# Kernel optimization log

Hardware: AMD Instinct MI355X
Metric: run time of the kernel (lower is better)

The kernel has to match this reference:

```python
import jax, jax.numpy as jnp
import numpy as np

D_TENSOR = 64  # matches init_kwargs; note: original divides scores by d_tensor (not sqrt)


def setup_inputs() -> dict:
    key = jax.random.key(0)
    kq, kk, kv = jax.random.split(key, 3)
    shape = (2, 12, 2048, 64)  # [B, H, S, D]
    return {
        "queries": jax.random.normal(kq, shape, dtype=jnp.float32),
        "keys": jax.random.normal(kk, shape, dtype=jnp.float32),
        "values": jax.random.normal(kv, shape, dtype=jnp.float32),
    }


def reference(queries, keys, values):
    # scores: [B, H, S, S]; faithful to source: divide by d_tensor (NOT sqrt)
    scores = jnp.einsum("bhqd,bhkd->bhqk", queries, keys) / D_TENSOR
    attn = jax.nn.softmax(scores, axis=-1)
    out = jnp.einsum("bhqk,bhkd->bhqd", attn, values)
    return (out, attn)
```

## Files before the change

kernel.cpp:

```cpp
#include <hip/hip_runtime.h>
#include <hip/hip_bf16.h>

namespace {

constexpr int S = 2048;
constexpr int D = 64;
constexpr int BH = 24;
constexpr int QT = 64;
constexpr int KT = 64;
constexpr int NKT = S / KT;
constexpr int PAD = 72;

typedef __attribute__((ext_vector_type(8))) __bf16 bf16x8;
typedef __attribute__((ext_vector_type(4))) __bf16 bf16x4;
typedef __attribute__((ext_vector_type(4))) float  f32x4;

__device__ inline bf16x4 cvt4(f32x4 f) {
    return __builtin_convertvector(f, bf16x4);
}

__global__ __launch_bounds__(256, 5)
void rowsum_kernel(const float* __restrict__ q,
                   const float* __restrict__ k,
                   float* __restrict__ invrs) {
    __shared__ unsigned short Ks[2][KT][PAD];
    __shared__ unsigned short QPs[QT][PAD];

    const int tid  = threadIdx.x;
    const int wid  = tid >> 6;
    const int lane = tid & 63;
    const int g    = lane >> 4;
    const int r16  = lane & 15;
    const int bh   = blockIdx.y;
    const int q0   = blockIdx.x * QT;

    const float* qg = q + ((size_t)bh * S + q0) * D;
    const float* kg = k + (size_t)bh * S * D;

    #pragma unroll
    for (int ii = 0; ii < 4; ++ii) {
        int idx = tid + ii * 256;
        int r = idx >> 4, c = (idx & 15) * 4;
        f32x4 f = *reinterpret_cast<const f32x4*>(qg + r * D + c);
        *reinterpret_cast<bf16x4*>(&QPs[r][c]) = cvt4(f);
    }
    __syncthreads();
    const bf16x8 bQ0 = *(const bf16x8*)&QPs[wid * 16 + r16][g * 8];
    const bf16x8 bQ1 = *(const bf16x8*)&QPs[wid * 16 + r16][32 + g * 8];

    float rs0 = 0.f, rs1 = 0.f;
    f32x4 pK[4];

    #pragma unroll
    for (int ii = 0; ii < 4; ++ii) {
        int idx = tid + ii * 256;
        int r = idx >> 4, c = (idx & 15) * 4;
        pK[ii] = *reinterpret_cast<const f32x4*>(kg + r * D + c);
    }
    #pragma unroll
    for (int ii = 0; ii < 4; ++ii) {
        int idx = tid + ii * 256;
        int r = idx >> 4, c = (idx & 15) * 4;
        *reinterpret_cast<bf16x4*>(&Ks[0][r][c]) = cvt4(pK[ii]);
    }
    __syncthreads();

    for (int t = 0; t < NKT; ++t) {
        const int cur = t & 1;
        if (t + 1 < NKT) {
            const float* ktg = kg + (size_t)(t + 1) * KT * D;
            #pragma unroll
            for (int ii = 0; ii < 4; ++ii) {
                int idx = tid + ii * 256;
                int r = idx >> 4, c = (idx & 15) * 4;
                pK[ii] = *reinterpret_cast<const f32x4*>(ktg + r * D + c);
            }
        }
        #pragma unroll
        for (int cf = 0; cf < 4; ++cf) {
            bf16x8 aK0 = *(const bf16x8*)&Ks[cur][cf * 16 + r16][g * 8];
            bf16x8 aK1 = *(const bf16x8*)&Ks[cur][cf * 16 + r16][32 + g * 8];
            f32x4 acc = {0.f, 0.f, 0.f, 0.f};
            acc = __builtin_amdgcn_mfma_f32_16x16x32_bf16(aK0, bQ0, acc, 0, 0, 0);
            acc = __builtin_amdgcn_mfma_f32_16x16x32_bf16(aK1, bQ1, acc, 0, 0, 0);
            rs0 += __expf(acc[0] * (1.0f / 64.0f)) + __expf(acc[2] * (1.0f / 64.0f));
            rs1 += __expf(acc[1] * (1.0f / 64.0f)) + __expf(acc[3] * (1.0f / 64.0f));
        }
        if (t + 1 < NKT) {
            const int nxt = (t + 1) & 1;
            #pragma unroll
            for (int ii = 0; ii < 4; ++ii) {
                int idx = tid + ii * 256;
                int r = idx >> 4, c = (idx & 15) * 4;
                *reinterpret_cast<bf16x4*>(&Ks[nxt][r][c]) = cvt4(pK[ii]);
            }
            __syncthreads();
        }
    }
    float rs = rs0 + rs1;
    rs += __shfl_xor(rs, 16, 64);
    rs += __shfl_xor(rs, 32, 64);
    if (lane < 16)
        invrs[(size_t)bh * S + q0 + wid * 16 + lane] = 1.0f / rs;
}

__global__ __launch_bounds__(256, 5)
void attn_pv_kernel(const float* __restrict__ q,
                    const float* __restrict__ k,
                    const float* __restrict__ v,
                    const float* __restrict__ invrs,
                    float* __restrict__ out,
                    float* __restrict__ attn) {
    __shared__ unsigned short Ks[KT][PAD];
    __shared__ unsigned short Vt[D][PAD];
    __shared__ unsigned short QPs[QT][PAD];

    const int tid  = threadIdx.x;
    const int wid  = tid >> 6;
    const int lane = tid & 63;
    const int g    = lane >> 4;
    const int r16  = lane & 15;
    const int bh   = blockIdx.y;
    const int q0   = blockIdx.x * QT;

    const float* qg = q + ((size_t)bh * S + q0) * D;
    const float* kg = k + (size_t)bh * S * D;
    const float* vg = v + (size_t)bh * S * D;
    float* attng = attn + ((size_t)bh * S + q0) * S;
    float* outg  = out  + ((size_t)bh * S + q0) * D;

    #pragma unroll
    for (int ii = 0; ii < 4; ++ii) {
        int idx = tid + ii * 256;
        int r = idx >> 4, c = (idx & 15) * 4;
        f32x4 f = *reinterpret_cast<const f32x4*>(qg + r * D + c);
        *reinterpret_cast<bf16x4*>(&QPs[r][c]) = cvt4(f);
    }
    __syncthreads();
    const bf16x8 bQ0 = *(const bf16x8*)&QPs[wid * 16 + r16][g * 8];
    const bf16x8 bQ1 = *(const bf16x8*)&QPs[wid * 16 + r16][32 + g * 8];

    const float inv = invrs[(size_t)bh * S + q0 + wid * 16 + r16];

    f32x4 oacc[4];
    #pragma unroll
    for (int n = 0; n < 4; ++n) oacc[n] = {0.f, 0.f, 0.f, 0.f};

    f32x4 pK[4], pV[4];
    const int vk0 = (tid & 15) * 4;
    const int vc  = (tid >> 4) * 4;

    #pragma unroll
    for (int ii = 0; ii < 4; ++ii) {
        int idx = tid + ii * 256;
        int r = idx >> 4, c = (idx & 15) * 4;
        pK[ii] = *reinterpret_cast<const f32x4*>(kg + r * D + c);
        pV[ii] = *reinterpret_cast<const f32x4*>(vg + (vk0 + ii) * D + vc);
    }
    #pragma unroll
    for (int ii = 0; ii < 4; ++ii) {
        int idx = tid + ii * 256;
        int r = idx >> 4, c = (idx & 15) * 4;
        *reinterpret_cast<bf16x4*>(&Ks[r][c]) = cvt4(pK[ii]);
    }
    #pragma unroll
    for (int j = 0; j < 4; ++j) {
        f32x4 col = { pV[0][j], pV[1][j], pV[2][j], pV[3][j] };
        *reinterpret_cast<bf16x4*>(&Vt[vc + j][vk0]) = cvt4(col);
    }
    __syncthreads();

    for (int t = 0; t < NKT; ++t) {
        if (t + 1 < NKT) {
            const float* ktg = kg + (size_t)(t + 1) * KT * D;
            const float* vtg = vg + (size_t)(t + 1) * KT * D;
            #pragma unroll
            for (int ii = 0; ii < 4; ++ii) {
                int idx = tid + ii * 256;
                int r = idx >> 4, c = (idx & 15) * 4;
                pK[ii] = *reinterpret_cast<const f32x4*>(ktg + r * D + c);
                pV[ii] = *reinterpret_cast<const f32x4*>(vtg + (vk0 + ii) * D + vc);
            }
        }
        #pragma unroll
        for (int cf = 0; cf < 4; ++cf) {
            bf16x8 aK0 = *(const bf16x8*)&Ks[cf * 16 + r16][g * 8];
            bf16x8 aK1 = *(const bf16x8*)&Ks[cf * 16 + r16][32 + g * 8];
            f32x4 acc = {0.f, 0.f, 0.f, 0.f};
            acc = __builtin_amdgcn_mfma_f32_16x16x32_bf16(aK0, bQ0, acc, 0, 0, 0);
            acc = __builtin_amdgcn_mfma_f32_16x16x32_bf16(aK1, bQ1, acc, 0, 0, 0);
            f32x4 pst;
            #pragma unroll
            for (int e = 0; e < 4; ++e)
                pst[e] = __expf(acc[e] * (1.0f / 64.0f)) * inv;
            __builtin_nontemporal_store(pst, reinterpret_cast<f32x4*>(
                attng + (size_t)(wid * 16 + r16) * S + t * KT + cf * 16 + g * 4));
            *reinterpret_cast<bf16x4*>(&QPs[wid * 16 + r16][cf * 16 + g * 4]) = cvt4(pst);
        }
        bf16x8 aP0 = *(const bf16x8*)&QPs[wid * 16 + r16][g * 8];
        bf16x8 aP1 = *(const bf16x8*)&QPs[wid * 16 + r16][32 + g * 8];
        #pragma unroll
        for (int n = 0; n < 4; ++n) {
            bf16x8 bv0 = *(const bf16x8*)&Vt[n * 16 + r16][g * 8];
            bf16x8 bv1 = *(const bf16x8*)&Vt[n * 16 + r16][32 + g * 8];
            oacc[n] = __builtin_amdgcn_mfma_f32_16x16x32_bf16(aP0, bv0, oacc[n], 0, 0, 0);
            oacc[n] = __builtin_amdgcn_mfma_f32_16x16x32_bf16(aP1, bv1, oacc[n], 0, 0, 0);
        }
        if (t + 1 < NKT) {
            __syncthreads();
            #pragma unroll
            for (int ii = 0; ii < 4; ++ii) {
                int idx = tid + ii * 256;
                int r = idx >> 4, c = (idx & 15) * 4;
                *reinterpret_cast<bf16x4*>(&Ks[r][c]) = cvt4(pK[ii]);
            }
            #pragma unroll
            for (int j = 0; j < 4; ++j) {
                f32x4 col = { pV[0][j], pV[1][j], pV[2][j], pV[3][j] };
                *reinterpret_cast<bf16x4*>(&Vt[vc + j][vk0]) = cvt4(col);
            }
            __syncthreads();
        }
    }

    #pragma unroll
    for (int n = 0; n < 4; ++n) {
        #pragma unroll
        for (int e = 0; e < 4; ++e) {
            __builtin_nontemporal_store(oacc[n][e],
                outg + (size_t)(wid * 16 + g * 4 + e) * D + n * 16 + r16);
        }
    }
}

__global__ __launch_bounds__(256, 3)
void sdpa_fallback(const float* __restrict__ q,
                   const float* __restrict__ k,
                   const float* __restrict__ v,
                   float* __restrict__ out,
                   float* __restrict__ attn) {
    __shared__ unsigned short Ks[2][KT][PAD];
    __shared__ unsigned short Vt[2][D][PAD];
    __shared__ unsigned short QPs[QT][PAD];

    const int tid  = threadIdx.x;
    const int wid  = tid >> 6;
    const int lane = tid & 63;
    const int g    = lane >> 4;
    const int r16  = lane & 15;
    const int bh   = blockIdx.y;
    const int q0   = blockIdx.x * QT;

    const float* qg = q + ((size_t)bh * S + q0) * D;
    const float* kg = k + (size_t)bh * S * D;
    const float* vg = v + (size_t)bh * S * D;
    float* attng = attn + ((size_t)bh * S + q0) * S;
    float* outg  = out  + ((size_t)bh * S + q0) * D;

    #pragma unroll
    for (int ii = 0; ii < 4; ++ii) {
        int idx = tid + ii * 256;
        int r = idx >> 4, c = (idx & 15) * 4;
        f32x4 f = *reinterpret_cast<const f32x4*>(qg + r * D + c);
        *reinterpret_cast<bf16x4*>(&QPs[r][c]) = cvt4(f);
    }
    __syncthreads();
    const bf16x8 bQ0 = *(const bf16x8*)&QPs[wid * 16 + r16][g * 8];
    const bf16x8 bQ1 = *(const bf16x8*)&QPs[wid * 16 + r16][32 + g * 8];

    float rs = 0.0f;
    f32x4 pK[4];

    #pragma unroll
    for (int ii = 0; ii < 4; ++ii) {
        int idx = tid + ii * 256;
        int r = idx >> 4, c = (idx & 15) * 4;
        pK[ii] = *reinterpret_cast<const f32x4*>(kg + r * D + c);
    }
    #pragma unroll
    for (int ii = 0; ii < 4; ++ii) {
        int idx = tid + ii * 256;
        int r = idx >> 4, c = (idx & 15) * 4;
        *reinterpret_cast<bf16x4*>(&Ks[0][r][c]) = cvt4(pK[ii]);
    }
    __syncthreads();

    for (int t = 0; t < NKT; ++t) {
        const int cur = t & 1;
        if (t + 1 < NKT) {
            const float* ktg = kg + (size_t)(t + 1) * KT * D;
            #pragma unroll
            for (int ii = 0; ii < 4; ++ii) {
                int idx = tid + ii * 256;
                int r = idx >> 4, c = (idx & 15) * 4;
                pK[ii] = *reinterpret_cast<const f32x4*>(ktg + r * D + c);
            }
        }
        #pragma unroll
        for (int cf = 0; cf < 4; ++cf) {
            bf16x8 aK0 = *(const bf16x8*)&Ks[cur][cf * 16 + r16][g * 8];
            bf16x8 aK1 = *(const bf16x8*)&Ks[cur][cf * 16 + r16][32 + g * 8];
            f32x4 acc = {0.f, 0.f, 0.f, 0.f};
            acc = __builtin_amdgcn_mfma_f32_16x16x32_bf16(aK0, bQ0, acc, 0, 0, 0);
            acc = __builtin_amdgcn_mfma_f32_16x16x32_bf16(aK1, bQ1, acc, 0, 0, 0);
            #pragma unroll
            for (int e = 0; e < 4; ++e)
                rs += __expf(acc[e] * (1.0f / 64.0f));
        }
        if (t + 1 < NKT) {
            const int nxt = (t + 1) & 1;
            #pragma unroll
            for (int ii = 0; ii < 4; ++ii) {
                int idx = tid + ii * 256;
                int r = idx >> 4, c = (idx & 15) * 4;
                *reinterpret_cast<bf16x4*>(&Ks[nxt][r][c]) = cvt4(pK[ii]);
            }
            __syncthreads();
        }
    }
    rs += __shfl_xor(rs, 16, 64);
    rs += __shfl_xor(rs, 32, 64);
    const float inv = 1.0f / rs;

    f32x4 oacc[4];
    #pragma unroll
    for (int n = 0; n < 4; ++n) oacc[n] = {0.f, 0.f, 0.f, 0.f};

    f32x4 pV[4];
    const int vk0 = (tid & 15) * 4;
    const int vc  = (tid >> 4) * 4;

    #pragma unroll
    for (int ii = 0; ii < 4; ++ii) {
        int idx = tid + ii * 256;
        int r = idx >> 4, c = (idx & 15) * 4;
        pK[ii] = *reinterpret_cast<const f32x4*>(kg + r * D + c);
        pV[ii] = *reinterpret_cast<const f32x4*>(vg + (vk0 + ii) * D + vc);
    }
    #pragma unroll
    for (int ii = 0; ii < 4; ++ii) {
        int idx = tid + ii * 256;
        int r = idx >> 4, c = (idx & 15) * 4;
        *reinterpret_cast<bf16x4*>(&Ks[0][r][c]) = cvt4(pK[ii]);
    }
    #pragma unroll
    for (int j = 0; j < 4; ++j) {
        f32x4 col = { pV[0][j], pV[1][j], pV[2][j], pV[3][j] };
        *reinterpret_cast<bf16x4*>(&Vt[0][vc + j][vk0]) = cvt4(col);
    }
    __syncthreads();

    for (int t = 0; t < NKT; ++t) {
        const int cur = t & 1;
        if (t + 1 < NKT) {
            const float* ktg = kg + (size_t)(t + 1) * KT * D;
            const float* vtg = vg + (size_t)(t + 1) * KT * D;
            #pragma unroll
            for (int ii = 0; ii < 4; ++ii) {
                int idx = tid + ii * 256;
                int r = idx >> 4, c = (idx & 15) * 4;
                pK[ii] = *reinterpret_cast<const f32x4*>(ktg + r * D + c);
                pV[ii] = *reinterpret_cast<const f32x4*>(vtg + (vk0 + ii) * D + vc);
            }
        }
        #pragma unroll
        for (int cf = 0; cf < 4; ++cf) {
            bf16x8 aK0 = *(const bf16x8*)&Ks[cur][cf * 16 + r16][g * 8];
            bf16x8 aK1 = *(const bf16x8*)&Ks[cur][cf * 16 + r16][32 + g * 8];
            f32x4 acc = {0.f, 0.f, 0.f, 0.f};
            acc = __builtin_amdgcn_mfma_f32_16x16x32_bf16(aK0, bQ0, acc, 0, 0, 0);
            acc = __builtin_amdgcn_mfma_f32_16x16x32_bf16(aK1, bQ1, acc, 0, 0, 0);
            f32x4 pst;
            #pragma unroll
            for (int e = 0; e < 4; ++e)
                pst[e] = __expf(acc[e] * (1.0f / 64.0f)) * inv;
            __builtin_nontemporal_store(pst, reinterpret_cast<f32x4*>(
                attng + (size_t)(wid * 16 + r16) * S + t * KT + cf * 16 + g * 4));
            *reinterpret_cast<bf16x4*>(&QPs[wid * 16 + r16][cf * 16 + g * 4]) = cvt4(pst);
        }
        bf16x8 aP0 = *(const bf16x8*)&QPs[wid * 16 + r16][g * 8];
        bf16x8 aP1 = *(const bf16x8*)&QPs[wid * 16 + r16][32 + g * 8];
        #pragma unroll
        for (int n = 0; n < 4; ++n) {
            bf16x8 bv0 = *(const bf16x8*)&Vt[cur][n * 16 + r16][g * 8];
            bf16x8 bv1 = *(const bf16x8*)&Vt[cur][n * 16 + r16][32 + g * 8];
            oacc[n] = __builtin_amdgcn_mfma_f32_16x16x32_bf16(aP0, bv0, oacc[n], 0, 0, 0);
            oacc[n] = __builtin_amdgcn_mfma_f32_16x16x32_bf16(aP1, bv1, oacc[n], 0, 0, 0);
        }
        if (t + 1 < NKT) {
            const int nxt = (t + 1) & 1;
            #pragma unroll
            for (int ii = 0; ii < 4; ++ii) {
                int idx = tid + ii * 256;
                int r = idx >> 4, c = (idx & 15) * 4;
                *reinterpret_cast<bf16x4*>(&Ks[nxt][r][c]) = cvt4(pK[ii]);
            }
            #pragma unroll
            for (int j = 0; j < 4; ++j) {
                f32x4 col = { pV[0][j], pV[1][j], pV[2][j], pV[3][j] };
                *reinterpret_cast<bf16x4*>(&Vt[nxt][vc + j][vk0]) = cvt4(col);
            }
            __syncthreads();
        }
    }

    #pragma unroll
    for (int n = 0; n < 4; ++n) {
        #pragma unroll
        for (int e = 0; e < 4; ++e) {
            __builtin_nontemporal_store(oacc[n][e],
                outg + (size_t)(wid * 16 + g * 4 + e) * D + n * 16 + r16);
        }
    }
}

}

extern "C" void kernel_launch(void* const* d_in, const int* in_sizes, int n_in,
                              void* d_out, int out_size, void* d_ws, size_t ws_size,
                              hipStream_t stream) {
    const float* q = (const float*)d_in[0];
    const float* k = (const float*)d_in[1];
    const float* v = (const float*)d_in[2];
    float* out  = (float*)d_out;
    float* attn = out + (size_t)BH * S * D;

    constexpr size_t RS_BYTES = (size_t)BH * S * sizeof(float);

    if (ws_size >= RS_BYTES) {
        float* invrs = (float*)d_ws;
        dim3 grid(S / QT, BH);
        rowsum_kernel<<<grid, 256, 0, stream>>>(q, k, invrs);
        attn_pv_kernel<<<grid, 256, 0, stream>>>(q, k, v, invrs, out, attn);
    } else {
        dim3 grid(S / QT, BH);
        sdpa_fallback<<<grid, 256, 0, stream>>>(q, k, v, out, attn);
    }
}
```

Measured before the change: 155.1 us.

## Split rowsum over key chunks, double-buffer PV, coalesce attn/out stores via LDS

The rowsum pass now splits the key dimension into four chunks across a z grid dimension and writes partial sums, which the attention pass combines. This gives the first pass more parallelism. The attention kernel double-buffers its K/V tiles, dropping one barrier per iteration. Attention probabilities are now written from LDS in row-contiguous 128-bit stores, and the output is staged through LDS for coalesced writes. The trade-offs are a lower occupancy target (launch bounds 3), more LDS, extra workspace, and attn values that are now bf16-rounded before being written.

After: 130.8 us. -15.6%, faster.

```diff
diff --git a/kernel.cpp b/kernel.cpp
--- a/kernel.cpp
+++ b/kernel.cpp
@@ -9,6 +9,9 @@
 constexpr int QT = 64;
 constexpr int KT = 64;
 constexpr int NKT = S / KT;
+constexpr int KSPLIT = 4;
+constexpr int SK = S / KSPLIT;
+constexpr int NKT2 = SK / KT;
 constexpr int PAD = 72;
 
 typedef __attribute__((ext_vector_type(8))) __bf16 bf16x8;
@@ -20,11 +23,11 @@
 }
 
 __global__ __launch_bounds__(256, 5)
-void rowsum_kernel(const float* __restrict__ q,
-                   const float* __restrict__ k,
-                   float* __restrict__ invrs) {
+void rowsum_partial(const float* __restrict__ q,
+                    const float* __restrict__ k,
+                    float* __restrict__ psum) {
     __shared__ unsigned short Ks[2][KT][PAD];
-    __shared__ unsigned short QPs[QT][PAD];
+    __shared__ unsigned short Qs[QT][PAD];
 
     const int tid  = threadIdx.x;
     const int wid  = tid >> 6;
@@ -33,20 +36,21 @@
     const int r16  = lane & 15;
     const int bh   = blockIdx.y;
     const int q0   = blockIdx.x * QT;
+    const int kz   = blockIdx.z;
 
     const float* qg = q + ((size_t)bh * S + q0) * D;
-    const float* kg = k + (size_t)bh * S * D;
+    const float* kg = k + ((size_t)bh * S + kz * SK) * D;
 
     #pragma unroll
     for (int ii = 0; ii < 4; ++ii) {
         int idx = tid + ii * 256;
         int r = idx >> 4, c = (idx & 15) * 4;
         f32x4 f = *reinterpret_cast<const f32x4*>(qg + r * D + c);
-        *reinterpret_cast<bf16x4*>(&QPs[r][c]) = cvt4(f);
-    }
-    __syncthreads();
-    const bf16x8 bQ0 = *(const bf16x8*)&QPs[wid * 16 + r16][g * 8];
-    const bf16x8 bQ1 = *(const bf16x8*)&QPs[wid * 16 + r16][32 + g * 8];
+        *reinterpret_cast<bf16x4*>(&Qs[r][c]) = cvt4(f);
+    }
+    __syncthreads();
+    const bf16x8 bQ0 = *(const bf16x8*)&Qs[wid * 16 + r16][g * 8];
+    const bf16x8 bQ1 = *(const bf16x8*)&Qs[wid * 16 + r16][32 + g * 8];
 
     float rs0 = 0.f, rs1 = 0.f;
     f32x4 pK[4];
@@ -65,9 +69,9 @@
     }
     __syncthreads();
 
-    for (int t = 0; t < NKT; ++t) {
+    for (int t = 0; t < NKT2; ++t) {
         const int cur = t & 1;
-        if (t + 1 < NKT) {
+        if (t + 1 < NKT2) {
             const float* ktg = kg + (size_t)(t + 1) * KT * D;
             #pragma unroll
             for (int ii = 0; ii < 4; ++ii) {
@@ -86,7 +90,7 @@
             rs0 += __expf(acc[0] * (1.0f / 64.0f)) + __expf(acc[2] * (1.0f / 64.0f));
             rs1 += __expf(acc[1] * (1.0f / 64.0f)) + __expf(acc[3] * (1.0f / 64.0f));
         }
-        if (t + 1 < NKT) {
+        if (t + 1 < NKT2) {
             const int nxt = (t + 1) & 1;
             #pragma unroll
             for (int ii = 0; ii < 4; ++ii) {
@@ -101,18 +105,18 @@
     rs += __shfl_xor(rs, 16, 64);
     rs += __shfl_xor(rs, 32, 64);
     if (lane < 16)
-        invrs[(size_t)bh * S + q0 + wid * 16 + lane] = 1.0f / rs;
-}
-
-__global__ __launch_bounds__(256, 5)
-void attn_pv_kernel(const float* __restrict__ q,
-                    const float* __restrict__ k,
-                    const float* __restrict__ v,
-                    const float* __restrict__ invrs,
-                    float* __restrict__ out,
-                    float* __restrict__ attn) {
-    __shared__ unsigned short Ks[KT][PAD];
-    __shared__ unsigned short Vt[D][PAD];
+        psum[((size_t)kz * BH + bh) * S + q0 + wid * 16 + lane] = rs;
+}
+
+__global__ __launch_bounds__(256, 3)
+void attn_pv(const float* __restrict__ q,
+             const float* __restrict__ k,
+             const float* __restrict__ v,
+             const float* __restrict__ psum,
+             float* __restrict__ out,
+             float* __restrict__ attn) {
+    __shared__ unsigned short Ks[2][KT][PAD];
+    __shared__ unsigned short Vt[2][D][PAD];
     __shared__ unsigned short QPs[QT][PAD];
 
     const int tid  = threadIdx.x;
@@ -120,6 +124,8 @@
     const int lane = tid & 63;
     const int g    = lane >> 4;
     const int r16  = lane & 15;
+    const int sr   = lane >> 3;
+    const int sc   = (lane & 7) * 4;
     const int bh   = blockIdx.y;
     const int q0   = blockIdx.x * QT;
 
@@ -140,7 +146,12 @@
     const bf16x8 bQ0 = *(const bf16x8*)&QPs[wid * 16 + r16][g * 8];
     const bf16x8 bQ1 = *(const bf16x8*)&QPs[wid * 16 + r16][32 + g * 8];
 
-    const float inv = invrs[(size_t)bh * S + q0 + wid * 16 + r16];
+    const size_t rowi = (size_t)bh * S + q0 + wid * 16 + r16;
+    const float p0 = psum[rowi];
+    const float p1 = psum[(size_t)BH * S + rowi];
+    const float p2 = psum[(size_t)2 * BH * S + rowi];
+    const float p3 = psum[(size_t)3 * BH * S + rowi];
+    const float inv = 1.0f / (((p0 + p1) + p2) + p3);
 
     f32x4 oacc[4];
     #pragma unroll
@@ -161,16 +172,17 @@
     for (int ii = 0; ii < 4; ++ii) {
         int idx = tid + ii * 256;
         int r = idx >> 4, c = (idx & 15) * 4;
-        *reinterpret_cast<bf16x4*>(&Ks[r][c]) = cvt4(pK[ii]);
+        *reinterpret_cast<bf16x4*>(&Ks[0][r][c]) = cvt4(pK[ii]);
     }
     #pragma unroll
     for (int j = 0; j < 4; ++j) {
         f32x4 col = { pV[0][j], pV[1][j], pV[2][j], pV[3][j] };
-        *reinterpret_cast<bf16x4*>(&Vt[vc + j][vk0]) = cvt4(col);
+        *reinterpret_cast<bf16x4*>(&Vt[0][vc + j][vk0]) = cvt4(col);
     }
     __syncthreads();
 
     for (int t = 0; t < NKT; ++t) {
+        const int cur = t & 1;
         if (t + 1 < NKT) {
             const float* ktg = kg + (size_t)(t + 1) * KT * D;
             const float* vtg = vg + (size_t)(t + 1) * KT * D;
@@ -184,8 +196,8 @@
         }
         #pragma unroll
         for (int cf = 0; cf < 4; ++cf) {
-            bf16x8 aK0 = *(const bf16x8*)&Ks[cf * 16 + r16][g * 8];
-            bf16x8 aK1 = *(const bf16x8*)&Ks[cf * 16 + r16][32 + g * 8];
+            bf16x8 aK0 = *(const bf16x8*)&Ks[cur][cf * 16 + r16][g * 8];
+            bf16x8 aK1 = *(const bf16x8*)&Ks[cur][cf * 16 + r16][32 + g * 8];
             f32x4 acc = {0.f, 0.f, 0.f, 0.f};
             acc = __builtin_amdgcn_mfma_f32_16x16x32_bf16(aK0, bQ0, acc, 0, 0, 0);
             acc = __builtin_amdgcn_mfma_f32_16x16x32_bf16(aK1, bQ1, acc, 0, 0, 0);
@@ -193,42 +205,63 @@
             #pragma unroll
             for (int e = 0; e < 4; ++e)
                 pst[e] = __expf(acc[e] * (1.0f / 64.0f)) * inv;
-            __builtin_nontemporal_store(pst, reinterpret_cast<f32x4*>(
-                attng + (size_t)(wid * 16 + r16) * S + t * KT + cf * 16 + g * 4));
             *reinterpret_cast<bf16x4*>(&QPs[wid * 16 + r16][cf * 16 + g * 4]) = cvt4(pst);
         }
         bf16x8 aP0 = *(const bf16x8*)&QPs[wid * 16 + r16][g * 8];
         bf16x8 aP1 = *(const bf16x8*)&QPs[wid * 16 + r16][32 + g * 8];
         #pragma unroll
         for (int n = 0; n < 4; ++n) {
-            bf16x8 bv0 = *(const bf16x8*)&Vt[n * 16 + r16][g * 8];
-            bf16x8 bv1 = *(const bf16x8*)&Vt[n * 16 + r16][32 + g * 8];
+            bf16x8 bv0 = *(const bf16x8*)&Vt[cur][n * 16 + r16][g * 8];
+            bf16x8 bv1 = *(const bf16x8*)&Vt[cur][n * 16 + r16][32 + g * 8];
             oacc[n] = __builtin_amdgcn_mfma_f32_16x16x32_bf16(aP0, bv0, oacc[n], 0, 0, 0);
             oacc[n] = __builtin_amdgcn_mfma_f32_16x16x32_bf16(aP1, bv1, oacc[n], 0, 0, 0);
         }
-        if (t + 1 < NKT) {
-            __syncthreads();
-            #pragma unroll
-            for (int ii = 0; ii < 4; ++ii) {
-                int idx = tid + ii * 256;
-                int r = idx >> 4, c = (idx & 15) * 4;
-                *reinterpret_cast<bf16x4*>(&Ks[r][c]) = cvt4(pK[ii]);
+        #pragma unroll
+        for (int h = 0; h < 2; ++h) {
+            const int row = wid * 16 + h * 8 + sr;
+            #pragma unroll
+            for (int half = 0; half < 2; ++half) {
+                bf16x4 pb = *reinterpret_cast<const bf16x4*>(&QPs[row][half * 32 + sc]);
+                f32x4 pf = __builtin_convertvector(pb, f32x4);
+                __builtin_nontemporal_store(pf, reinterpret_cast<f32x4*>(
+                    attng + (size_t)row * S + t * KT + half * 32 + sc));
+            }
+        }
+        if (t + 1 < NKT) {
+            const int nxt = (t + 1) & 1;
+            #pragma unroll
+            for (int ii = 0; ii < 4; ++ii) {
+                int idx = tid + ii * 256;
+                int r = idx >> 4, c = (idx & 15) * 4;
+                *reinterpret_cast<bf16x4*>(&Ks[nxt][r][c]) = cvt4(pK[ii]);
             }
             #pragma unroll
             for (int j = 0; j < 4; ++j) {
                 f32x4 col = { pV[0][j], pV[1][j], pV[2][j], pV[3][j] };
-                *reinterpret_cast<bf16x4*>(&Vt[vc + j][vk0]) = cvt4(col);
+                *reinterpret_cast<bf16x4*>(&Vt[nxt][vc + j][vk0]) = cvt4(col);
             }
             __syncthreads();
         }
     }
 
+    __syncthreads();
+    float* KsF = reinterpret_cast<float*>(&Ks[0][0][0]);
     #pragma unroll
     for (int n = 0; n < 4; ++n) {
         #pragma unroll
         for (int e = 0; e < 4; ++e) {
-            __builtin_nontemporal_store(oacc[n][e],
-                outg + (size_t)(wid * 16 + g * 4 + e) * D + n * 16 + r16);
+            KsF[(wid * 16 + g * 4 + e) * 72 + n * 16 + r16] = oacc[n][e];
+        }
+    }
+    __syncthreads();
+    #pragma unroll
+    for (int h = 0; h < 2; ++h) {
+        const int row = wid * 16 + h * 8 + sr;
+        #pragma unroll
+        for (int half = 0; half < 2; ++half) {
+            f32x4 o = *reinterpret_cast<const f32x4*>(&KsF[row * 72 + half * 32 + sc]);
+            __builtin_nontemporal_store(o, reinterpret_cast<f32x4*>(
+                outg + (size_t)row * D + half * 32 + sc));
         }
     }
 }
@@ -248,6 +281,8 @@
     const int lane = tid & 63;
     const int g    = lane >> 4;
     const int r16  = lane & 15;
+    const int sr   = lane >> 3;
+    const int sc   = (lane & 7) * 4;
     const int bh   = blockIdx.y;
     const int q0   = blockIdx.x * QT;
 
@@ -374,8 +409,6 @@
             #pragma unroll
             for (int e = 0; e < 4; ++e)
                 pst[e] = __expf(acc[e] * (1.0f / 64.0f)) * inv;
-            __builtin_nontemporal_store(pst, reinterpret_cast<f32x4*>(
-                attng + (size_t)(wid * 16 + r16) * S + t * KT + cf * 16 + g * 4));
             *reinterpret_cast<bf16x4*>(&QPs[wid * 16 + r16][cf * 16 + g * 4]) = cvt4(pst);
         }
         bf16x8 aP0 = *(const bf16x8*)&QPs[wid * 16 + r16][g * 8];
@@ -387,6 +420,17 @@
             oacc[n] = __builtin_amdgcn_mfma_f32_16x16x32_bf16(aP0, bv0, oacc[n], 0, 0, 0);
             oacc[n] = __builtin_amdgcn_mfma_f32_16x16x32_bf16(aP1, bv1, oacc[n], 0, 0, 0);
         }
+        #pragma unroll
+        for (int h = 0; h < 2; ++h) {
+            const int row = wid * 16 + h * 8 + sr;
+            #pragma unroll
+            for (int half = 0; half < 2; ++half) {
+                bf16x4 pb = *reinterpret_cast<const bf16x4*>(&QPs[row][half * 32 + sc]);
+                f32x4 pf = __builtin_convertvector(pb, f32x4);
+                __builtin_nontemporal_store(pf, reinterpret_cast<f32x4*>(
+                    attng + (size_t)row * S + t * KT + half * 32 + sc));
+            }
+        }
         if (t + 1 < NKT) {
             const int nxt = (t + 1) & 1;
             #pragma unroll
@@ -404,12 +448,24 @@
         }
     }
 
+    __syncthreads();
+    float* KsF = reinterpret_cast<float*>(&Ks[0][0][0]);
     #pragma unroll
     for (int n = 0; n < 4; ++n) {
         #pragma unroll
         for (int e = 0; e < 4; ++e) {
-            __builtin_nontemporal_store(oacc[n][e],
-                outg + (size_t)(wid * 16 + g * 4 + e) * D + n * 16 + r16);
+            KsF[(wid * 16 + g * 4 + e) * 72 + n * 16 + r16] = oacc[n][e];
+        }
+    }
+    __syncthreads();
+    #pragma unroll
+    for (int h = 0; h < 2; ++h) {
+        const int row = wid * 16 + h * 8 + sr;
+        #pragma unroll
+        for (int half = 0; half < 2; ++half) {
+            f32x4 o = *reinterpret_cast<const f32x4*>(&KsF[row * 72 + half * 32 + sc]);
+            __builtin_nontemporal_store(o, reinterpret_cast<f32x4*>(
+                outg + (size_t)row * D + half * 32 + sc));
         }
     }
 }
@@ -425,15 +481,13 @@
     float* out  = (float*)d_out;
     float* attn = out + (size_t)BH * S * D;
 
-    constexpr size_t RS_BYTES = (size_t)BH * S * sizeof(float);
-
-    if (ws_size >= RS_BYTES) {
-        float* invrs = (float*)d_ws;
-        dim3 grid(S / QT, BH);
-        rowsum_kernel<<<grid, 256, 0, stream>>>(q, k, invrs);
-        attn_pv_kernel<<<grid, 256, 0, stream>>>(q, k, v, invrs, out, attn);
+    constexpr size_t PS_BYTES = (size_t)KSPLIT * BH * S * sizeof(float);
+
+    if (ws_size >= PS_BYTES) {
+        float* psum = (float*)d_ws;
+        rowsum_partial<<<dim3(S / QT, BH, KSPLIT), 256, 0, stream>>>(q, k, psum);
+        attn_pv<<<dim3(S / QT, BH), 256, 0, stream>>>(q, k, v, psum, out, attn);
     } else {
-        dim3 grid(S / QT, BH);
-        sdpa_fallback<<<grid, 256, 0, stream>>>(q, k, v, out, attn);
-    }
-}
+        sdpa_fallback<<<dim3(S / QT, BH), 256, 0, stream>>>(q, k, v, out, attn);
+    }
+}
```
